# Performance work log

Hardware: AMD Instinct MI355X
Metric: run time of the kernel (lower is better)

## Reference

```python
import jax, jax.numpy as jnp
import numpy as np

B, D, C = 512, 256, 100000
M, S, T = 0.2, 30.0, 1.0
EPS = 1e-12


def _l2norm(x, axis):
    n = jnp.sqrt(jnp.sum(x * x, axis=axis, keepdims=True))
    return x / jnp.maximum(n, EPS)


def setup_inputs() -> dict:
    key = jax.random.key(0)
    ks = jax.random.split(key, 7)
    inputs = jax.random.normal(ks[0], (B, D, 1), dtype=jnp.float32)
    weight = 0.01 * jax.random.normal(ks[1], (C, D), dtype=jnp.float32)
    lam = jax.random.uniform(ks[2], (), dtype=jnp.float32)
    targets1 = jax.random.randint(ks[3], (B,), 0, C)
    pre1 = jax.random.randint(ks[4], (B,), 0, C)
    targets2 = jax.random.randint(ks[5], (B,), 0, C)
    pre2 = jax.random.randint(ks[6], (B,), 0, C)
    return {"inputs": inputs, "weight": weight, "lam": lam,
            "targets1": targets1, "pre1": pre1,
            "targets2": targets2, "pre2": pre2}


def reference(inputs, weight, lam, targets1, pre1, targets2, pre2):
    # inputs: [B, D, 1] -> squeeze frame dim
    x = _l2norm(inputs[:, :, 0], axis=1)          # [B, D]
    w = _l2norm(weight, axis=1)                   # [C, D]
    cos = jnp.einsum('bd,cd->bc', x, w)           # [B, C] cosine similarities
    rows = jnp.arange(B)

    # AM-softmax penalty (lambda_factor = 0 -> penalty = cos - m)
    pen_t1 = cos[rows, targets1] - M
    pen_p1 = cos[rows, pre1] - M
    pen_t2 = cos[rows, targets2] - M
    pen_p2 = cos[rows, pre2] - M

    # Faithful to torch source: targets1 penalty scattered BEFORE scaling by s,
    # the other three scattered AFTER (hence unscaled), same overwrite order.
    out = S * cos.at[rows, targets1].set(pen_t1)
    out = out.at[rows, pre1].set(pen_p1)
    out = out.at[rows, targets2].set(pen_t2)
    out = out.at[rows, pre2].set(pen_p2)

    lsm = jax.nn.log_softmax(out / T, axis=1)     # [B, C]
    ce = lambda tgt: -jnp.mean(lsm[rows, tgt])
    loss = lam * (0.2 * ce(targets1) + 0.8 * ce(pre1)) \
         + (1.0 - lam) * (0.2 * ce(targets2) + 0.8 * ce(pre2))
    return loss
```

## Files before the change

kernel.cpp:

```cpp
#include <hip/hip_runtime.h>
#include <stdint.h>

#define DDIM 256
#define BROWS 512
#define CCOLS 100000
#define NCHUNK 3125
#define MM 0.2f
#define SS 30.0f

typedef __attribute__((ext_vector_type(8))) short bf16x8;
typedef __attribute__((ext_vector_type(16))) float f32x16;

__device__ __forceinline__ float b2f(unsigned short u) {
    union { unsigned int i; float f; } v; v.i = ((unsigned int)u) << 16; return v.f;
}
__device__ __forceinline__ unsigned short f2b(float f) {
    union { float f; unsigned int i; } v; v.f = f;
    unsigned int r = v.i + 0x7FFFu + ((v.i >> 16) & 1u);
    return (unsigned short)(r >> 16);
}

__global__ void norm_rows(const float* __restrict__ src, unsigned short* __restrict__ dst, int nrows) {
    int row = blockIdx.x * (blockDim.x >> 6) + (threadIdx.x >> 6);
    if (row >= nrows) return;
    int lane = threadIdx.x & 63;
    float4 v = ((const float4*)(src + (size_t)row * DDIM))[lane];
    float ss = v.x * v.x + v.y * v.y + v.z * v.z + v.w * v.w;
#pragma unroll
    for (int m = 1; m <= 32; m <<= 1) ss += __shfl_xor(ss, m);
    float inv = 1.0f / fmaxf(sqrtf(ss), 1e-12f);
    ushort4 o;
    o.x = f2b(v.x * inv); o.y = f2b(v.y * inv); o.z = f2b(v.z * inv); o.w = f2b(v.w * inv);
    ((ushort4*)(dst + (size_t)row * DDIM))[lane] = o;
}

__global__ __launch_bounds__(256) void gemm_lse(const unsigned short* __restrict__ xn,
                                                const unsigned short* __restrict__ wn,
                                                float* __restrict__ sums ) {
    int p    = blockIdx.x;
    int lane = threadIdx.x & 63;
    int wave = threadIdx.x >> 6;
    int colh = lane & 31;
    int kg   = (lane >> 5) * 8;

    size_t col = (size_t)p * 32 + colh;
    const unsigned short* wbase = wn + col * DDIM + kg;
    bf16x8 bfrag[16];
#pragma unroll
    for (int kk = 0; kk < 16; ++kk)
        bfrag[kk] = *(const bf16x8*)(wbase + kk * 16);

    int rbase = wave * 128 + 4 * (lane >> 5);
    const unsigned short* xbase = xn + (size_t)(wave * 128 + colh) * DDIM + kg;

#pragma unroll
    for (int rt = 0; rt < 4; ++rt) {
        f32x16 acc;
#pragma unroll
        for (int i = 0; i < 16; ++i) acc[i] = 0.0f;
        const unsigned short* xr = xbase + (size_t)rt * 32 * DDIM;
#pragma unroll
        for (int kk = 0; kk < 16; ++kk) {
            bf16x8 af = *(const bf16x8*)(xr + kk * 16);
            acc = __builtin_amdgcn_mfma_f32_32x32x16_bf16(af, bfrag[kk], acc, 0, 0, 0);
        }
#pragma unroll
        for (int r = 0; r < 16; ++r) {
            float e = __expf(SS * acc[r]);
#pragma unroll
            for (int m = 1; m <= 16; m <<= 1) e += __shfl_xor(e, m);
            if (colh == 0) {
                int row = rbase + rt * 32 + (r & 3) + 8 * (r >> 2);
                sums[(size_t)row * NCHUNK + p] = e;
            }
        }
    }
}

__global__ void row_reduce(const float* __restrict__ sums, float* __restrict__ rowsum) {
    int b = blockIdx.x;
    float s = 0.0f;
    for (int i = threadIdx.x; i < NCHUNK; i += 256) s += sums[(size_t)b * NCHUNK + i];
#pragma unroll
    for (int m = 1; m <= 32; m <<= 1) s += __shfl_xor(s, m);
    __shared__ float ls[4];
    if ((threadIdx.x & 63) == 0) ls[threadIdx.x >> 6] = s;
    __syncthreads();
    if (threadIdx.x == 0) rowsum[b] = ls[0] + ls[1] + ls[2] + ls[3];
}

__global__ void finalize(const unsigned short* __restrict__ xn,
                         const unsigned short* __restrict__ wn,
                         const float* __restrict__ rowsum,
                         const float* __restrict__ lamp,
                         const int* __restrict__ t1, const int* __restrict__ p1,
                         const int* __restrict__ t2, const int* __restrict__ p2,
                         float* __restrict__ out) {
    int b = blockIdx.x * (blockDim.x >> 6) + (threadIdx.x >> 6);
    int lane = threadIdx.x & 63;
    ushort4 xr = ((const ushort4*)(xn + (size_t)b * DDIM))[lane];
    float x0 = b2f(xr.x), x1 = b2f(xr.y), x2 = b2f(xr.z), x3 = b2f(xr.w);
    int idx[4] = { t1[b], p1[b], t2[b], p2[b] };
    float cosv[4];
#pragma unroll
    for (int k = 0; k < 4; ++k) {
        ushort4 wr = ((const ushort4*)(wn + (size_t)idx[k] * DDIM))[lane];
        float s = x0 * b2f(wr.x) + x1 * b2f(wr.y) + x2 * b2f(wr.z) + x3 * b2f(wr.w);
#pragma unroll
        for (int m = 1; m <= 32; m <<= 1) s += __shfl_xor(s, m);
        cosv[k] = s;
    }
    if (lane == 0) {
        auto finalv = [&](int k) -> float {
            int c = idx[k]; float cv = cosv[k];
            if (c == idx[3]) return cv - MM;
            if (c == idx[2]) return cv - MM;
            if (c == idx[1]) return cv - MM;
            return SS * (cv - MM);
        };
        float delta = 0.0f;
#pragma unroll
        for (int k = 0; k < 4; ++k) {
            bool first = true;
            for (int j = 0; j < k; ++j) if (idx[j] == idx[k]) first = false;
            if (first) delta += __expf(finalv(k)) - __expf(SS * cosv[k]);
        }
        float lse = logf(rowsum[b] + delta);
        float lam = lamp[0];
        float lossb = lam        * (0.2f * (lse - finalv(0)) + 0.8f * (lse - finalv(1)))
                    + (1.f - lam) * (0.2f * (lse - finalv(2)) + 0.8f * (lse - finalv(3)));
        atomicAdd(out, lossb * (1.0f / 512.0f));
    }
}

extern "C" void kernel_launch(void* const* d_in, const int* in_sizes, int n_in,
                              void* d_out, int out_size, void* d_ws, size_t ws_size,
                              hipStream_t stream) {
    const float* x   = (const float*)d_in[0];
    const float* w   = (const float*)d_in[1];
    const float* lam = (const float*)d_in[2];
    const int* t1    = (const int*)d_in[3];
    const int* p1    = (const int*)d_in[4];
    const int* t2    = (const int*)d_in[5];
    const int* p2    = (const int*)d_in[6];
    float* out = (float*)d_out;

    char* ws = (char*)d_ws;
    unsigned short* xn = (unsigned short*)ws;
    unsigned short* wn = (unsigned short*)(ws + 262144);
    float* sums   = (float*)(ws + 262144 + 51200000);
    float* rowsum = (float*)(ws + 262144 + 51200000 + 6400000);

    hipMemsetAsync(out, 0, sizeof(float), stream);
    norm_rows<<<128,   256, 0, stream>>>(x, xn, BROWS);
    norm_rows<<<25000, 256, 0, stream>>>(w, wn, CCOLS);
    gemm_lse<<<NCHUNK, 256, 0, stream>>>(xn, wn, sums);
    row_reduce<<<BROWS, 256, 0, stream>>>(sums, rowsum);
    finalize<<<128, 256, 0, stream>>>(xn, wn, rowsum, lam, t1, p1, t2, p2, out);
}
```

Baseline: 313.8 us.

## Fuse weight normalization into GEMM and merge reduce with finalize

Weight-row L2 normalization and bf16 conversion now happen inside the GEMM block, which stages the 128 normalized columns in shared memory. This removes the separate pass that wrote and reread a 51MB bf16 weight copy. The x operand is pre-packed into MFMA fragment order, each wave computes eight 32x32 tiles, and the per-chunk exp sums are reduced inside registers before being written. The row reduction is merged with the finalize step, which recomputes the target cosines from the fp32 inputs. The cost is higher register pressure with eight f32x16 accumulators and a 64-float staging array per thread, plus an LDS dependency at the start of each block.

```diff
diff --git a/kernel.cpp b/kernel.cpp
--- a/kernel.cpp
+++ b/kernel.cpp
@@ -4,7 +4,8 @@
 #define DDIM 256
 #define BROWS 512
 #define CCOLS 100000
-#define NCHUNK 3125
+#define NBLK 782
+#define NCH  (NBLK * 4)
 #define MM 0.2f
 #define SS 30.0f
 
@@ -20,116 +21,155 @@
     return (unsigned short)(r >> 16);
 }
 
-__global__ void norm_rows(const float* __restrict__ src, unsigned short* __restrict__ dst, int nrows) {
-    int row = blockIdx.x * (blockDim.x >> 6) + (threadIdx.x >> 6);
-    if (row >= nrows) return;
-    int lane = threadIdx.x & 63;
-    float4 v = ((const float4*)(src + (size_t)row * DDIM))[lane];
+__global__ void norm_x_pack(const float* __restrict__ x, unsigned short* __restrict__ xp) {
+    int row = blockIdx.x * 4 + (threadIdx.x >> 6);
+    int ln  = threadIdx.x & 63;
+    float4 v = ((const float4*)(x + (size_t)row * DDIM))[ln];
     float ss = v.x * v.x + v.y * v.y + v.z * v.z + v.w * v.w;
 #pragma unroll
     for (int m = 1; m <= 32; m <<= 1) ss += __shfl_xor(ss, m);
     float inv = 1.0f / fmaxf(sqrtf(ss), 1e-12f);
+    int g = row >> 5, n = row & 31;
+    int kk = ln >> 2, hi = (ln >> 1) & 1;
+    size_t uoff = ((size_t)(g * 16 + kk) * 64 + hi * 32 + n) * 8 + (ln & 1) * 4;
     ushort4 o;
     o.x = f2b(v.x * inv); o.y = f2b(v.y * inv); o.z = f2b(v.z * inv); o.w = f2b(v.w * inv);
-    ((ushort4*)(dst + (size_t)row * DDIM))[lane] = o;
+    *(ushort4*)(xp + uoff) = o;
 }
 
-__global__ __launch_bounds__(256) void gemm_lse(const unsigned short* __restrict__ xn,
-                                                const unsigned short* __restrict__ wn,
-                                                float* __restrict__ sums ) {
-    int p    = blockIdx.x;
-    int lane = threadIdx.x & 63;
-    int wave = threadIdx.x >> 6;
-    int colh = lane & 31;
-    int kg   = (lane >> 5) * 8;
+__global__ __launch_bounds__(512, 2) void fused_gemm(const float* __restrict__ w,
+                                                     const unsigned short* __restrict__ xp,
+                                                     float* __restrict__ sums) {
+    __shared__ unsigned short wlds[16 * 2 * 128 * 8];
+    int blk = blockIdx.x, t = threadIdx.x;
+    int cbase = blk * 128;
 
-    size_t col = (size_t)p * 32 + colh;
-    const unsigned short* wbase = wn + col * DDIM + kg;
-    bf16x8 bfrag[16];
+    {
+        int col = t >> 2, q = t & 3;
+        int gcol = cbase + col;
+        float f[64];
+        if (gcol < CCOLS) {
+            const float4* src = (const float4*)(w + (size_t)gcol * DDIM + q * 64);
 #pragma unroll
-    for (int kk = 0; kk < 16; ++kk)
-        bfrag[kk] = *(const bf16x8*)(wbase + kk * 16);
+            for (int i = 0; i < 16; ++i) {
+                float4 v = src[i];
+                f[i * 4 + 0] = v.x; f[i * 4 + 1] = v.y; f[i * 4 + 2] = v.z; f[i * 4 + 3] = v.w;
+            }
+        } else {
+#pragma unroll
+            for (int i = 0; i < 64; ++i) f[i] = 0.0f;
+        }
+        float ss = 0.0f;
+#pragma unroll
+        for (int i = 0; i < 64; ++i) ss += f[i] * f[i];
+        ss += __shfl_xor(ss, 1); ss += __shfl_xor(ss, 2);
+        float inv = 1.0f / fmaxf(sqrtf(ss), 1e-12f);
+#pragma unroll
+        for (int s = 0; s < 8; ++s) {
+            int kk = q * 4 + (s >> 1), hi = s & 1;
+            int o = (s >> 1) * 16 + (s & 1) * 8;
+            unsigned int u0 = (unsigned)f2b(f[o+0]*inv) | ((unsigned)f2b(f[o+1]*inv) << 16);
+            unsigned int u1 = (unsigned)f2b(f[o+2]*inv) | ((unsigned)f2b(f[o+3]*inv) << 16);
+            unsigned int u2 = (unsigned)f2b(f[o+4]*inv) | ((unsigned)f2b(f[o+5]*inv) << 16);
+            unsigned int u3 = (unsigned)f2b(f[o+6]*inv) | ((unsigned)f2b(f[o+7]*inv) << 16);
+            uint4 pk = make_uint4(u0, u1, u2, u3);
+            *(uint4*)(wlds + (size_t)((kk * 2 + hi) * 128 + col) * 8) = pk;
+        }
+    }
+    __syncthreads();
 
-    int rbase = wave * 128 + 4 * (lane >> 5);
-    const unsigned short* xbase = xn + (size_t)(wave * 128 + colh) * DDIM + kg;
+    int wv = t >> 6, lane = t & 63;
+    int rg = wv >> 2, cg = wv & 3;
+    int m = lane & 31, hi = lane >> 5;
 
+    f32x16 acc[8];
 #pragma unroll
-    for (int rt = 0; rt < 4; ++rt) {
-        f32x16 acc;
+    for (int rs = 0; rs < 8; ++rs)
 #pragma unroll
-        for (int i = 0; i < 16; ++i) acc[i] = 0.0f;
-        const unsigned short* xr = xbase + (size_t)rt * 32 * DDIM;
+        for (int i = 0; i < 16; ++i) acc[rs][i] = 0.0f;
+
+#pragma unroll 4
+    for (int kk = 0; kk < 16; ++kk) {
+        bf16x8 wf = *(const bf16x8*)(wlds + (size_t)((kk * 2 + hi) * 128 + cg * 32 + m) * 8);
 #pragma unroll
-        for (int kk = 0; kk < 16; ++kk) {
-            bf16x8 af = *(const bf16x8*)(xr + kk * 16);
-            acc = __builtin_amdgcn_mfma_f32_32x32x16_bf16(af, bfrag[kk], acc, 0, 0, 0);
+        for (int rs = 0; rs < 8; ++rs) {
+            bf16x8 xf = *(const bf16x8*)(xp + ((size_t)((rg * 8 + rs) * 16 + kk) * 64 + lane) * 8);
+            acc[rs] = __builtin_amdgcn_mfma_f32_32x32x16_bf16(wf, xf, acc[rs], 0, 0, 0);
         }
+    }
+
+    int colb = cbase + cg * 32;
+#pragma unroll
+    for (int rs = 0; rs < 8; ++rs) {
+        float p = 0.0f;
 #pragma unroll
         for (int r = 0; r < 16; ++r) {
-            float e = __expf(SS * acc[r]);
-#pragma unroll
-            for (int m = 1; m <= 16; m <<= 1) e += __shfl_xor(e, m);
-            if (colh == 0) {
-                int row = rbase + rt * 32 + (r & 3) + 8 * (r >> 2);
-                sums[(size_t)row * NCHUNK + p] = e;
-            }
+            int cl = (r & 3) + 8 * (r >> 2) + 4 * hi;
+            float e = __expf(SS * acc[rs][r]);
+            p += (colb + cl < CCOLS) ? e : 0.0f;
+        }
+        p += __shfl_xor(p, 32);
+        if (hi == 0) {
+            int row = rg * 256 + rs * 32 + m;
+            sums[(size_t)row * NCH + blk * 4 + cg] = p;
         }
     }
 }
 
-__global__ void row_reduce(const float* __restrict__ sums, float* __restrict__ rowsum) {
-    int b = blockIdx.x;
+__global__ void reduce_finalize(const float* __restrict__ sums,
+                                const float* __restrict__ x, const float* __restrict__ w,
+                                const float* __restrict__ lamp,
+                                const int* __restrict__ t1, const int* __restrict__ p1,
+                                const int* __restrict__ t2, const int* __restrict__ p2,
+                                float* __restrict__ out) {
+    int b = blockIdx.x, t = threadIdx.x;
     float s = 0.0f;
-    for (int i = threadIdx.x; i < NCHUNK; i += 256) s += sums[(size_t)b * NCHUNK + i];
+    for (int i = t; i < NCH; i += 256) s += sums[(size_t)b * NCH + i];
 #pragma unroll
     for (int m = 1; m <= 32; m <<= 1) s += __shfl_xor(s, m);
     __shared__ float ls[4];
-    if ((threadIdx.x & 63) == 0) ls[threadIdx.x >> 6] = s;
+    if ((t & 63) == 0) ls[t >> 6] = s;
     __syncthreads();
-    if (threadIdx.x == 0) rowsum[b] = ls[0] + ls[1] + ls[2] + ls[3];
-}
-
-__global__ void finalize(const unsigned short* __restrict__ xn,
-                         const unsigned short* __restrict__ wn,
-                         const float* __restrict__ rowsum,
-                         const float* __restrict__ lamp,
-                         const int* __restrict__ t1, const int* __restrict__ p1,
-                         const int* __restrict__ t2, const int* __restrict__ p2,
-                         float* __restrict__ out) {
-    int b = blockIdx.x * (blockDim.x >> 6) + (threadIdx.x >> 6);
-    int lane = threadIdx.x & 63;
-    ushort4 xr = ((const ushort4*)(xn + (size_t)b * DDIM))[lane];
-    float x0 = b2f(xr.x), x1 = b2f(xr.y), x2 = b2f(xr.z), x3 = b2f(xr.w);
-    int idx[4] = { t1[b], p1[b], t2[b], p2[b] };
-    float cosv[4];
+    if (t < 64) {
+        int ln = t;
+        float rowsum = ls[0] + ls[1] + ls[2] + ls[3];
+        float4 xv = ((const float4*)(x + (size_t)b * DDIM))[ln];
+        float ssx = xv.x*xv.x + xv.y*xv.y + xv.z*xv.z + xv.w*xv.w;
 #pragma unroll
-    for (int k = 0; k < 4; ++k) {
-        ushort4 wr = ((const ushort4*)(wn + (size_t)idx[k] * DDIM))[lane];
-        float s = x0 * b2f(wr.x) + x1 * b2f(wr.y) + x2 * b2f(wr.z) + x3 * b2f(wr.w);
-#pragma unroll
-        for (int m = 1; m <= 32; m <<= 1) s += __shfl_xor(s, m);
-        cosv[k] = s;
-    }
-    if (lane == 0) {
-        auto finalv = [&](int k) -> float {
-            int c = idx[k]; float cv = cosv[k];
-            if (c == idx[3]) return cv - MM;
-            if (c == idx[2]) return cv - MM;
-            if (c == idx[1]) return cv - MM;
-            return SS * (cv - MM);
-        };
-        float delta = 0.0f;
+        for (int m = 1; m <= 32; m <<= 1) ssx += __shfl_xor(ssx, m);
+        float xinv = 1.0f / fmaxf(sqrtf(ssx), 1e-12f);
+        int idx[4] = { t1[b], p1[b], t2[b], p2[b] };
+        float cosv[4];
 #pragma unroll
         for (int k = 0; k < 4; ++k) {
-            bool first = true;
-            for (int j = 0; j < k; ++j) if (idx[j] == idx[k]) first = false;
-            if (first) delta += __expf(finalv(k)) - __expf(SS * cosv[k]);
+            float4 wv = ((const float4*)(w + (size_t)idx[k] * DDIM))[ln];
+            float d  = xv.x*wv.x + xv.y*wv.y + xv.z*wv.z + xv.w*wv.w;
+            float sw = wv.x*wv.x + wv.y*wv.y + wv.z*wv.z + wv.w*wv.w;
+#pragma unroll
+            for (int m = 1; m <= 32; m <<= 1) { d += __shfl_xor(d, m); sw += __shfl_xor(sw, m); }
+            cosv[k] = d * xinv / fmaxf(sqrtf(sw), 1e-12f);
         }
-        float lse = logf(rowsum[b] + delta);
-        float lam = lamp[0];
-        float lossb = lam        * (0.2f * (lse - finalv(0)) + 0.8f * (lse - finalv(1)))
-                    + (1.f - lam) * (0.2f * (lse - finalv(2)) + 0.8f * (lse - finalv(3)));
-        atomicAdd(out, lossb * (1.0f / 512.0f));
+        if (ln == 0) {
+            auto finalv = [&](int k) -> float {
+                int c = idx[k]; float cv = cosv[k];
+                if (c == idx[3]) return cv - MM;
+                if (c == idx[2]) return cv - MM;
+                if (c == idx[1]) return cv - MM;
+                return SS * (cv - MM);
+            };
+            float delta = 0.0f;
+#pragma unroll
+            for (int k = 0; k < 4; ++k) {
+                bool first = true;
+                for (int j = 0; j < k; ++j) if (idx[j] == idx[k]) first = false;
+                if (first) delta += __expf(finalv(k)) - __expf(SS * cosv[k]);
+            }
+            float lse = logf(rowsum + delta);
+            float lam = lamp[0];
+            float lossb = lam          * (0.2f * (lse - finalv(0)) + 0.8f * (lse - finalv(1)))
+                        + (1.0f - lam) * (0.2f * (lse - finalv(2)) + 0.8f * (lse - finalv(3)));
+            atomicAdd(out, lossb * (1.0f / 512.0f));
+        }
     }
 }
 
@@ -146,15 +186,11 @@
     float* out = (float*)d_out;
 
     char* ws = (char*)d_ws;
-    unsigned short* xn = (unsigned short*)ws;
-    unsigned short* wn = (unsigned short*)(ws + 262144);
-    float* sums   = (float*)(ws + 262144 + 51200000);
-    float* rowsum = (float*)(ws + 262144 + 51200000 + 6400000);
+    unsigned short* xpack = (unsigned short*)ws;
+    float* sums = (float*)(ws + 262144);
 
     hipMemsetAsync(out, 0, sizeof(float), stream);
-    norm_rows<<<128,   256, 0, stream>>>(x, xn, BROWS);
-    norm_rows<<<25000, 256, 0, stream>>>(w, wn, CCOLS);
-    gemm_lse<<<NCHUNK, 256, 0, stream>>>(xn, wn, sums);
-    row_reduce<<<BROWS, 256, 0, stream>>>(sums, rowsum);
-    finalize<<<128, 256, 0, stream>>>(xn, wn, rowsum, lam, t1, p1, t2, p2, out);
+    norm_x_pack<<<128, 256, 0, stream>>>(x, xpack);
+    fused_gemm<<<NBLK, 512, 0, stream>>>(w, xpack, sums);
+    reduce_finalize<<<BROWS, 256, 0, stream>>>(sums, x, w, lam, t1, p1, t2, p2, out);
 }
```

Result: faster. 305.5 us (-2.6%).
